# Kernel optimization log

Measured on AMD Instinct MI355X. Metric: run time of the kernel, lower is better.

## Reference

```python
import jax, jax.numpy as jnp
import numpy as np

B, C, L = 8, 512, 2048   # batch, input_dim (channels), sequence length
H = 8                    # multihead_cnt
K = 3                    # kernel_dim
DH = C // H              # per-head dim = 64
SCALE = 1.0 / float(np.sqrt(C))  # module divides by sqrt(input_dim), not sqrt(head_dim)


def _conv1d(x, w, b):
    # x: [B, C, L], w: [C_out, C_in, K], padding=1 keeps L
    y = jax.lax.conv_general_dilated(x, w, window_strides=(1,), padding=[(1, 1)],
                                     dimension_numbers=('NCH', 'OIH', 'NCH'))
    return y + b[None, :, None]


def setup_inputs() -> dict:
    key = jax.random.key(0)
    ks = jax.random.split(key, 7)
    x = jax.random.normal(ks[0], (B, C, L), dtype=jnp.float32)
    # xavier_normal_ std for Conv1d weight [C, C, K]: sqrt(2 / (fan_in + fan_out)), fan = C*K
    std = float(np.sqrt(2.0 / (C * K + C * K)))
    inp = {'x': x}
    for i in range(3):  # conv_cnt = 3 -> q, k, v convolutions
        inp[f'w{i}'] = jax.random.normal(ks[1 + 2 * i], (C, C, K), dtype=jnp.float32) * std
        inp[f'b{i}'] = jax.random.normal(ks[2 + 2 * i], (C,), dtype=jnp.float32) * 0.01
    return inp


def reference(x, w0, b0, w1, b1, w2, b2):
    # q, k, v projections via Conv1d (padding preserves length)
    q = _conv1d(x, w0, b0)  # [B, C, L]
    k = _conv1d(x, w1, b1)
    v = _conv1d(x, w2, b2)
    # torch.chunk along dim 1 == contiguous reshape into heads
    qh = q.reshape(B, H, DH, L)
    kh = k.reshape(B, H, DH, L)
    vh = v.reshape(B, H, DH, L)
    # scores = q^T k / sqrt(input_dim)  -> [B, H, L, L]
    scores = jnp.einsum('bhdl,bhdm->bhlm', qh, kh) * SCALE
    att = jax.nn.softmax(scores, axis=-1)
    # out = (att @ v^T)^T -> [B, H, DH, L]
    out = jnp.einsum('bhlm,bhdm->bhdl', att, vh)
    return out.reshape(B, C, L)
```

## Files before the change

kernel.cpp:

```cpp
#include <hip/hip_runtime.h>
#include <hip/hip_bf16.h>
#include <cstdint>

typedef unsigned short u16;
typedef short v8s __attribute__((ext_vector_type(8)));
typedef float v4f __attribute__((ext_vector_type(4)));
typedef u16 u16x8 __attribute__((ext_vector_type(8)));
typedef u16 u16x4 __attribute__((ext_vector_type(4)));

static constexpr int Bb = 8, Cc = 512, Ll = 2048, Hh = 8, Dh = 64;

__device__ __forceinline__ float bf2f(u16 u){
  unsigned x = ((unsigned)u) << 16; float f; __builtin_memcpy(&f, &x, 4); return f;
}
__device__ __forceinline__ u16 f2bf(float f){
  unsigned x; __builtin_memcpy(&x, &f, 4);
  x = (x + 0x7fffu + ((x >> 16) & 1u)) >> 16; return (u16)x;
}

__device__ __forceinline__ void async_cp16(const u16* g, u16* l){
  __builtin_amdgcn_global_load_lds(
      (const __attribute__((address_space(1))) unsigned int*)g,
      (__attribute__((address_space(3))) unsigned int*)l, 16, 0, 0);
}

#if __has_builtin(__builtin_amdgcn_exp2f)
#define EXP2F(x) __builtin_amdgcn_exp2f(x)
#else
#define EXP2F(x) exp2f(x)
#endif

__global__ __launch_bounds__(256) void detect_dtype(const u16* __restrict__ x, unsigned* __restrict__ flag){
  __shared__ int cnt;
  if (threadIdx.x == 0) cnt = 0;
  __syncthreads();
  int sane = 0;
  for (int i = threadIdx.x; i < 4096; i += 256){
    unsigned e = (x[2 * i] >> 7) & 0xFFu;
    sane += (e >= 90u && e <= 160u) ? 1 : 0;
  }
  atomicAdd(&cnt, sane);
  __syncthreads();
  if (threadIdx.x == 0) *flag = (cnt < 2458) ? 1u : 0u;
}

__global__ __launch_bounds__(256) void transpose_pad(const void* __restrict__ xv, const unsigned* __restrict__ flagp,
                                                     u16* __restrict__ xT){
  int b = blockIdx.z, ci0 = blockIdx.y * 64, l0 = blockIdx.x * 64;
  __shared__ u16 tb[64 * 72];
  const unsigned isf32 = *flagp;
  int t = threadIdx.x;
  int row = t >> 3, seg = t & 7;
  if (isf32){
    const float* xf = (const float*)xv;
    #pragma unroll
    for (int rnd = 0; rnd < 2; rnd++){
      int ci = row + rnd * 32;
      size_t off = ((size_t)(b * Cc + ci0 + ci)) * Ll + l0 + seg * 8;
      v4f a = *(const v4f*)(xf + off);
      v4f c4 = *(const v4f*)(xf + off + 4);
      #pragma unroll
      for (int j = 0; j < 4; j++) tb[(seg * 8 + j) * 72 + ci] = f2bf(a[j]);
      #pragma unroll
      for (int j = 0; j < 4; j++) tb[(seg * 8 + 4 + j) * 72 + ci] = f2bf(c4[j]);
    }
  } else {
    const u16* x = (const u16*)xv;
    #pragma unroll
    for (int rnd = 0; rnd < 2; rnd++){
      int ci = row + rnd * 32;
      u16x8 v = *(const u16x8*)(x + ((size_t)(b * Cc + ci0 + ci)) * Ll + l0 + seg * 8);
      #pragma unroll
      for (int j = 0; j < 8; j++) tb[(seg * 8 + j) * 72 + ci] = v[j];
    }
  }
  __syncthreads();
  #pragma unroll
  for (int rnd = 0; rnd < 2; rnd++){
    int l = row + rnd * 32;
    u16x8 v = *(const u16x8*)&tb[l * 72 + seg * 8];
    *(u16x8*)(xT + ((size_t)b * 2050 + 1 + l0 + l) * Cc + ci0 + seg * 8) = v;
  }
}

__global__ __launch_bounds__(256) void pack_w(const void* __restrict__ w0, const void* __restrict__ w1,
                                              const void* __restrict__ w2, const unsigned* __restrict__ flagp,
                                              u16* __restrict__ wp){
  int g = blockIdx.x * 256 + threadIdx.x;
  int ci = g & 511, co = (g >> 9) & 511, kc = g >> 18;
  int conv = kc / 3, k = kc - conv * 3;
  const void* w = (conv == 0) ? w0 : ((conv == 1) ? w1 : w2);
  size_t idx = (size_t)co * 1536 + ci * 3 + k;
  if (*flagp) wp[g] = f2bf(((const float*)w)[idx]);
  else        wp[g] = ((const u16*)w)[idx];
}

__global__ __launch_bounds__(256) void pack_b(const void* __restrict__ b0, const void* __restrict__ b1,
                                              const void* __restrict__ b2, const unsigned* __restrict__ flagp,
                                              u16* __restrict__ bb){
  int g = blockIdx.x * 256 + threadIdx.x;
  if (g >= 1536) return;
  int conv = g >> 9, c = g & 511;
  const void* bsrc = (conv == 0) ? b0 : ((conv == 1) ? b1 : b2);
  if (*flagp) bb[g] = f2bf(((const float*)bsrc)[c]);
  else        bb[g] = ((const u16*)bsrc)[c];
}

__global__ __launch_bounds__(256) void conv_gemm_fused(const u16* __restrict__ wp, const u16* __restrict__ xT,
                                                       const u16* __restrict__ bb, u16* __restrict__ qT,
                                                       u16* __restrict__ kT, u16* __restrict__ vN){
  int b = blockIdx.y, bx = blockIdx.x;
  int mt = bx >> 4, nt = bx & 15;
  int m0 = mt * 128, n0 = nt * 128;
  int conv = m0 >> 9;
  int co0 = m0 & 511;
  __shared__ u16 lA[3 * 128 * 32];
  __shared__ u16 lB[130 * 32];
  int t = threadIdx.x, wave = t >> 6, lane = t & 63, quad = lane >> 4, lid = lane & 15;
  int wm = (wave >> 1) * 64, wn = (wave & 1) * 64;
  v4f acc[4][4] = {};
  const size_t xbase = (size_t)b * 2050 * Cc;

  for (int it = 0; it < 16; it++){
    int ci0 = it << 5;
    #pragma unroll
    for (int r = 0; r < 2; r++){
      int e = (r * 256 + t) * 8;
      int row = e >> 5, cio = e & 31;
      async_cp16(xT + xbase + (size_t)(n0 + row) * 512 + ci0 + cio, &lB[e]);
    }
    #pragma unroll
    for (int r = 0; r < 6; r++){
      int e = (r * 256 + t) * 8;
      int ks = e >> 12, rem = e & 4095, row = rem >> 5, cio = rem & 31;
      async_cp16(wp + ((size_t)((conv * 3 + ks) * 512 + co0 + row)) * 512 + ci0 + cio, &lA[e]);
    }
    if (t < 8){
      int hr = 128 + (t >> 2), cio = (t & 3) * 8;
      u16x8 hv = *(const u16x8*)(xT + xbase + (size_t)(n0 + hr) * 512 + ci0 + cio);
      *(u16x8*)&lB[hr * 32 + cio] = hv;
    }
    __syncthreads();
    #pragma unroll
    for (int ks = 0; ks < 3; ks++){
      v8s aF[4], bF[4];
      #pragma unroll
      for (int i = 0; i < 4; i++) aF[i] = *(const v8s*)&lA[ks * 4096 + (wm + i * 16 + lid) * 32 + quad * 8];
      #pragma unroll
      for (int j = 0; j < 4; j++) bF[j] = *(const v8s*)&lB[(wn + j * 16 + lid + ks) * 32 + quad * 8];
      #pragma unroll
      for (int i = 0; i < 4; i++)
        #pragma unroll
        for (int j = 0; j < 4; j++)
          acc[i][j] = __builtin_amdgcn_mfma_f32_16x16x32_bf16(aF[i], bF[j], acc[i][j], 0, 0, 0);
    }
    __syncthreads();
  }

  const float qsc = (float)(1.4426950408889634 / 22.627416997969522);
  #pragma unroll
  for (int i = 0; i < 4; i++){
    int cog = m0 + wm + i * 16 + quad * 4;
    float bv[4];
    #pragma unroll
    for (int r = 0; r < 4; r++) bv[r] = bf2f(bb[cog + r]);
    #pragma unroll
    for (int j = 0; j < 4; j++){
      int l = n0 + wn + j * 16 + lid;
      if (conv < 2){
        int co = cog & 511;
        u16* dst = (conv == 0) ? qT : kT;
        u16x4 pk;
        #pragma unroll
        for (int r = 0; r < 4; r++){
          float v = acc[i][j][r] + bv[r];
          if (conv == 0) v *= qsc;
          pk[r] = f2bf(v);
        }
        *(u16x4*)(dst + ((((size_t)b * Hh + (co >> 6)) * Ll + l) << 6) + (co & 63)) = pk;
      } else {
        int co = cog - 1024;
        #pragma unroll
        for (int r = 0; r < 4; r++)
          vN[(((size_t)b * Cc + co + r) << 11) + l] = f2bf(acc[i][j][r] + bv[r]);
      }
    }
  }
}

__global__ __launch_bounds__(256) void attn_kernel(const u16* __restrict__ qT, const u16* __restrict__ kT,
                                                   const u16* __restrict__ vN, const unsigned* __restrict__ flagp,
                                                   void* __restrict__ outv){
  int bhx = blockIdx.x;
  int b = bhx >> 3, h = bhx & 7, l0 = blockIdx.y * 128;
  int t = threadIdx.x, w = t >> 6, lane = t & 63, quad = lane >> 4, lid = lane & 15;
  __shared__ u16 kls[128 * 72];
  __shared__ u16 vls[64 * 136];
  __shared__ float al[128];
  const unsigned isf32 = *flagp;
  const size_t bh = (size_t)b * Hh + h;

  v8s qF[2][2];
  #pragma unroll
  for (int ci = 0; ci < 2; ci++)
    #pragma unroll
    for (int ks = 0; ks < 2; ks++)
      qF[ci][ks] = *(const v8s*)(qT + ((bh * Ll) + l0 + w * 32 + ci * 16 + lid) * 64 + ks * 32 + quad * 8);

  v4f o[2][4] = {};
  float lsum[2] = {0.f, 0.f};

  for (int mt = 0; mt < 16; mt++){
    int m0 = mt * 128;
    {
      int row = t >> 3, seg = t & 7;
      #pragma unroll
      for (int rnd = 0; rnd < 4; rnd++){
        int m = row + rnd * 32;
        int slot = (m & ~31) | ((m & 4) << 2) | ((m & 24) >> 1) | (m & 3);
        u16x8 v = *(const u16x8*)(kT + (bh * Ll + m0 + m) * 64 + seg * 8);
        *(u16x8*)&kls[slot * 72 + seg * 8] = v;
      }
      int vrow = t >> 4, vseg = t & 15;
      #pragma unroll
      for (int rnd = 0; rnd < 4; rnd++){
        int d = vrow + rnd * 16;
        u16x8 v = *(const u16x8*)(vN + ((size_t)(b * Cc + h * Dh + d)) * Ll + m0 + vseg * 8);
        *(u16x8*)&vls[d * 136 + vseg * 8] = v;
      }
    }
    __syncthreads();

    v4f s[4][2][2] = {};
    #pragma unroll
    for (int ks = 0; ks < 2; ks++){
      v8s aF[4][2];
      #pragma unroll
      for (int c = 0; c < 4; c++)
        #pragma unroll
        for (int tt = 0; tt < 2; tt++)
          aF[c][tt] = *(const v8s*)&kls[(c * 32 + tt * 16 + lid) * 72 + ks * 32 + quad * 8];
      #pragma unroll
      for (int c = 0; c < 4; c++)
        #pragma unroll
        for (int tt = 0; tt < 2; tt++){
          s[c][tt][0] = __builtin_amdgcn_mfma_f32_16x16x32_bf16(aF[c][tt], qF[0][ks], s[c][tt][0], 0, 0, 0);
          s[c][tt][1] = __builtin_amdgcn_mfma_f32_16x16x32_bf16(aF[c][tt], qF[1][ks], s[c][tt][1], 0, 0, 0);
        }
    }

    #pragma unroll
    for (int c = 0; c < 4; c++){
      v8s aP[2];
      #pragma unroll
      for (int ci = 0; ci < 2; ci++){
        float p[8];
        #pragma unroll
        for (int tt = 0; tt < 2; tt++)
          #pragma unroll
          for (int r = 0; r < 4; r++){
            float e = EXP2F(s[c][tt][ci][r]);
            p[tt * 4 + r] = e;
            lsum[ci] += e;
          }
        unsigned u[4];
        #pragma unroll
        for (int k2 = 0; k2 < 4; k2++){
          __hip_bfloat162 hb = __float22bfloat162_rn(make_float2(p[2 * k2], p[2 * k2 + 1]));
          __builtin_memcpy(&u[k2], &hb, 4);
        }
        __builtin_memcpy(&aP[ci], u, 16);
      }
      v8s bV[4];
      #pragma unroll
      for (int df = 0; df < 4; df++)
        bV[df] = *(const v8s*)&vls[(df * 16 + lid) * 136 + c * 32 + quad * 8];
      #pragma unroll
      for (int ci = 0; ci < 2; ci++)
        #pragma unroll
        for (int df = 0; df < 4; df++)
          o[ci][df] = __builtin_amdgcn_mfma_f32_16x16x32_bf16(aP[ci], bV[df], o[ci][df], 0, 0, 0);
    }
    __syncthreads();
  }

  #pragma unroll
  for (int ci = 0; ci < 2; ci++){
    lsum[ci] += __shfl_xor(lsum[ci], 16);
    lsum[ci] += __shfl_xor(lsum[ci], 32);
  }
  if (quad == 0){
    al[w * 32 + lid] = 1.f / lsum[0];
    al[w * 32 + 16 + lid] = 1.f / lsum[1];
  }
  __syncthreads();
  #pragma unroll
  for (int lf = 0; lf < 2; lf++){
    v4f nv = *(const v4f*)&al[w * 32 + lf * 16 + quad * 4];
    #pragma unroll
    for (int df = 0; df < 4; df++){
      int d = df * 16 + lid;
      int l = l0 + w * 32 + lf * 16 + quad * 4;
      size_t ofs = (((bh << 6) + d) << 11) + l;
      if (isf32){
        v4f st;
        #pragma unroll
        for (int r = 0; r < 4; r++) st[r] = o[lf][df][r] * nv[r];
        *(v4f*)((float*)outv + ofs) = st;
      } else {
        u16x4 pk;
        #pragma unroll
        for (int r = 0; r < 4; r++) pk[r] = f2bf(o[lf][df][r] * nv[r]);
        *(u16x4*)((u16*)outv + ofs) = pk;
      }
    }
  }
}

extern "C" void kernel_launch(void* const* d_in, const int* in_sizes, int n_in,
                              void* d_out, int out_size, void* d_ws, size_t ws_size,
                              hipStream_t stream){
  const void* x  = d_in[0];
  const void* w0 = d_in[1];
  const void* b0 = d_in[2];
  const void* w1 = d_in[3];
  const void* b1 = d_in[4];
  const void* w2 = d_in[5];
  const void* b2 = d_in[6];
  u16* ws = (u16*)d_ws;
  unsigned* flag = (unsigned*)ws;
  u16* xT = ws + 64;
  u16* wp = xT + (size_t)8 * 2050 * 512;
  u16* bb = wp + (size_t)9 * 512 * 512;
  u16* qT = bb + 1536;
  u16* kT = qT + (size_t)8 * 8 * 2048 * 64;
  u16* vN = kT + (size_t)8 * 8 * 2048 * 64;

  detect_dtype<<<1, 256, 0, stream>>>((const u16*)x, flag);
  (void)hipMemsetAsync(xT, 0, (size_t)8 * 2050 * 512 * 2, stream);
  transpose_pad<<<dim3(32, 8, 8), 256, 0, stream>>>(x, flag, xT);
  pack_w<<<dim3(9 * 512 * 512 / 256), 256, 0, stream>>>(w0, w1, w2, flag, wp);
  pack_b<<<dim3(6), 256, 0, stream>>>(b0, b1, b2, flag, bb);
  conv_gemm_fused<<<dim3(192, 8), 256, 0, stream>>>(wp, xT, bb, qT, kT, vN);
  attn_kernel<<<dim3(64, 16), 256, 0, stream>>>(qT, kT, vN, flag, d_out);
}
```

Baseline: 321.8 us.

## Widen conv GEMM tile, async-load attention K/V, compute row sums via MFMA

Several changes land at once. The full-buffer memset is replaced by zeroing only the two pad rows inside transpose_pad, and the weight and bias pack kernels are merged into one launch. The conv GEMM N-tile doubles to 256 and the V output is staged through LDS for coalesced stores. The attention kernel loads K and V with global_load_lds async copies and computes softmax row sums with an extra MFMA against a ones vector instead of scalar adds and shuffles. This cuts launches, redundant memory traffic and VALU work, at the cost of higher register pressure in the GEMM and extra MFMA issue in attention.

```diff
diff --git a/kernel.cpp b/kernel.cpp
--- a/kernel.cpp
+++ b/kernel.cpp
@@ -81,50 +81,59 @@
     u16x8 v = *(const u16x8*)&tb[l * 72 + seg * 8];
     *(u16x8*)(xT + ((size_t)b * 2050 + 1 + l0 + l) * Cc + ci0 + seg * 8) = v;
   }
-}
-
-__global__ __launch_bounds__(256) void pack_w(const void* __restrict__ w0, const void* __restrict__ w1,
-                                              const void* __restrict__ w2, const unsigned* __restrict__ flagp,
-                                              u16* __restrict__ wp){
+  if (blockIdx.x == 0 && t < 8){
+    u16x8 z = {};
+    *(u16x8*)(xT + ((size_t)b * 2050 + 0) * Cc + ci0 + t * 8) = z;
+  }
+  if (blockIdx.x == 31 && t < 8){
+    u16x8 z = {};
+    *(u16x8*)(xT + ((size_t)b * 2050 + 2049) * Cc + ci0 + t * 8) = z;
+  }
+}
+
+__global__ __launch_bounds__(256) void pack_wb(const void* __restrict__ w0, const void* __restrict__ w1,
+                                               const void* __restrict__ w2, const void* __restrict__ b0,
+                                               const void* __restrict__ b1, const void* __restrict__ b2,
+                                               const unsigned* __restrict__ flagp,
+                                               u16* __restrict__ wp, u16* __restrict__ bb){
   int g = blockIdx.x * 256 + threadIdx.x;
-  int ci = g & 511, co = (g >> 9) & 511, kc = g >> 18;
-  int conv = kc / 3, k = kc - conv * 3;
-  const void* w = (conv == 0) ? w0 : ((conv == 1) ? w1 : w2);
-  size_t idx = (size_t)co * 1536 + ci * 3 + k;
-  if (*flagp) wp[g] = f2bf(((const float*)w)[idx]);
-  else        wp[g] = ((const u16*)w)[idx];
-}
-
-__global__ __launch_bounds__(256) void pack_b(const void* __restrict__ b0, const void* __restrict__ b1,
-                                              const void* __restrict__ b2, const unsigned* __restrict__ flagp,
-                                              u16* __restrict__ bb){
-  int g = blockIdx.x * 256 + threadIdx.x;
-  if (g >= 1536) return;
-  int conv = g >> 9, c = g & 511;
-  const void* bsrc = (conv == 0) ? b0 : ((conv == 1) ? b1 : b2);
-  if (*flagp) bb[g] = f2bf(((const float*)bsrc)[c]);
-  else        bb[g] = ((const u16*)bsrc)[c];
+  const unsigned isf32 = *flagp;
+  if (g < 9 * 512 * 512){
+    int ci = g & 511, co = (g >> 9) & 511, kc = g >> 18;
+    int conv = kc / 3, k = kc - conv * 3;
+    const void* w = (conv == 0) ? w0 : ((conv == 1) ? w1 : w2);
+    size_t idx = (size_t)co * 1536 + ci * 3 + k;
+    wp[g] = isf32 ? f2bf(((const float*)w)[idx]) : ((const u16*)w)[idx];
+  } else {
+    int g2 = g - 9 * 512 * 512;
+    if (g2 < 1536){
+      int conv = g2 >> 9, c = g2 & 511;
+      const void* bsrc = (conv == 0) ? b0 : ((conv == 1) ? b1 : b2);
+      bb[g2] = isf32 ? f2bf(((const float*)bsrc)[c]) : ((const u16*)bsrc)[c];
+    }
+  }
 }
 
 __global__ __launch_bounds__(256) void conv_gemm_fused(const u16* __restrict__ wp, const u16* __restrict__ xT,
                                                        const u16* __restrict__ bb, u16* __restrict__ qT,
                                                        u16* __restrict__ kT, u16* __restrict__ vN){
   int b = blockIdx.y, bx = blockIdx.x;
-  int mt = bx >> 4, nt = bx & 15;
-  int m0 = mt * 128, n0 = nt * 128;
+  int mt = bx >> 3, nt = bx & 7;
+  int m0 = mt * 128, n0 = nt * 256;
   int conv = m0 >> 9;
   int co0 = m0 & 511;
-  __shared__ u16 lA[3 * 128 * 32];
-  __shared__ u16 lB[130 * 32];
+  __shared__ u16 smem[12288 + 8256];
+  u16* lA = smem;
+  u16* lB = smem + 12288;
   int t = threadIdx.x, wave = t >> 6, lane = t & 63, quad = lane >> 4, lid = lane & 15;
-  int wm = (wave >> 1) * 64, wn = (wave & 1) * 64;
-  v4f acc[4][4] = {};
+  int wm = (wave >> 1) * 64, wn = (wave & 1) * 128;
+  v4f acc[4][8] = {};
   const size_t xbase = (size_t)b * 2050 * Cc;
 
   for (int it = 0; it < 16; it++){
     int ci0 = it << 5;
     #pragma unroll
-    for (int r = 0; r < 2; r++){
+    for (int r = 0; r < 4; r++){
       int e = (r * 256 + t) * 8;
       int row = e >> 5, cio = e & 31;
       async_cp16(xT + xbase + (size_t)(n0 + row) * 512 + ci0 + cio, &lB[e]);
@@ -136,40 +145,40 @@
       async_cp16(wp + ((size_t)((conv * 3 + ks) * 512 + co0 + row)) * 512 + ci0 + cio, &lA[e]);
     }
     if (t < 8){
-      int hr = 128 + (t >> 2), cio = (t & 3) * 8;
+      int hr = 256 + (t >> 2), cio = (t & 3) * 8;
       u16x8 hv = *(const u16x8*)(xT + xbase + (size_t)(n0 + hr) * 512 + ci0 + cio);
       *(u16x8*)&lB[hr * 32 + cio] = hv;
     }
     __syncthreads();
     #pragma unroll
     for (int ks = 0; ks < 3; ks++){
-      v8s aF[4], bF[4];
+      v8s aF[4], bF[8];
       #pragma unroll
       for (int i = 0; i < 4; i++) aF[i] = *(const v8s*)&lA[ks * 4096 + (wm + i * 16 + lid) * 32 + quad * 8];
       #pragma unroll
-      for (int j = 0; j < 4; j++) bF[j] = *(const v8s*)&lB[(wn + j * 16 + lid + ks) * 32 + quad * 8];
+      for (int j = 0; j < 8; j++) bF[j] = *(const v8s*)&lB[(wn + j * 16 + lid + ks) * 32 + quad * 8];
       #pragma unroll
       for (int i = 0; i < 4; i++)
         #pragma unroll
-        for (int j = 0; j < 4; j++)
+        for (int j = 0; j < 8; j++)
           acc[i][j] = __builtin_amdgcn_mfma_f32_16x16x32_bf16(aF[i], bF[j], acc[i][j], 0, 0, 0);
     }
     __syncthreads();
   }
 
   const float qsc = (float)(1.4426950408889634 / 22.627416997969522);
-  #pragma unroll
-  for (int i = 0; i < 4; i++){
-    int cog = m0 + wm + i * 16 + quad * 4;
-    float bv[4];
-    #pragma unroll
-    for (int r = 0; r < 4; r++) bv[r] = bf2f(bb[cog + r]);
-    #pragma unroll
-    for (int j = 0; j < 4; j++){
-      int l = n0 + wn + j * 16 + lid;
-      if (conv < 2){
-        int co = cog & 511;
-        u16* dst = (conv == 0) ? qT : kT;
+  if (conv < 2){
+    u16* dst = (conv == 0) ? qT : kT;
+    #pragma unroll
+    for (int i = 0; i < 4; i++){
+      int cog = m0 + wm + i * 16 + quad * 4;
+      float bv[4];
+      #pragma unroll
+      for (int r = 0; r < 4; r++) bv[r] = bf2f(bb[cog + r]);
+      int co = cog & 511;
+      #pragma unroll
+      for (int j = 0; j < 8; j++){
+        int l = n0 + wn + j * 16 + lid;
         u16x4 pk;
         #pragma unroll
         for (int r = 0; r < 4; r++){
@@ -178,11 +187,36 @@
           pk[r] = f2bf(v);
         }
         *(u16x4*)(dst + ((((size_t)b * Hh + (co >> 6)) * Ll + l) << 6) + (co & 63)) = pk;
-      } else {
-        int co = cog - 1024;
-        #pragma unroll
-        for (int r = 0; r < 4; r++)
-          vN[(((size_t)b * Cc + co + r) << 11) + l] = f2bf(acc[i][j][r] + bv[r]);
+      }
+    }
+  } else {
+    u16* scr = smem;
+    #pragma unroll
+    for (int cs = 0; cs < 2; cs++){
+      __syncthreads();
+      #pragma unroll
+      for (int i = 0; i < 4; i++){
+        int cog = m0 + wm + i * 16 + quad * 4;
+        float bv[4];
+        #pragma unroll
+        for (int r = 0; r < 4; r++) bv[r] = bf2f(bb[cog + r]);
+        #pragma unroll
+        for (int j = 0; j < 4; j++){
+          int jj = cs * 4 + j;
+          int lcl = (wave & 1) * 64 + j * 16 + lid;
+          #pragma unroll
+          for (int r = 0; r < 4; r++)
+            scr[(wm + i * 16 + quad * 4 + r) * 130 + lcl] = f2bf(acc[i][jj][r] + bv[r]);
+        }
+      }
+      __syncthreads();
+      int row = t & 127, half = t >> 7;
+      int co = co0 + row;
+      size_t gb = (((size_t)b * Cc + co) << 11) + n0 + half * 128 + cs * 64;
+      #pragma unroll
+      for (int s = 0; s < 8; s++){
+        u16x8 vv = *(const u16x8*)&scr[row * 130 + half * 64 + s * 8];
+        *(u16x8*)(vN + gb + s * 8) = vv;
       }
     }
   }
@@ -196,9 +230,25 @@
   int t = threadIdx.x, w = t >> 6, lane = t & 63, quad = lane >> 4, lid = lane & 15;
   __shared__ u16 kls[128 * 72];
   __shared__ u16 vls[64 * 136];
-  __shared__ float al[128];
   const unsigned isf32 = *flagp;
   const size_t bh = (size_t)b * Hh + h;
+
+  int kadd[5], vadd[5];
+  bool kval[5], vval[5];
+  #pragma unroll
+  for (int r = 0; r < 5; r++){
+    int e = (r * 256 + t) * 8;
+    kval[r] = e < 128 * 72;
+    int slot = e / 72, off = e - slot * 72;
+    int s5 = slot & 31;
+    int m = (slot & ~31) | (((s5 >> 2) & 1) << 3) | (((s5 >> 3) & 1) << 4) | (((s5 >> 4) & 1) << 2) | (s5 & 3);
+    kadd[r] = m * 64 + (off < 64 ? off : 0);
+    vval[r] = e < 64 * 136;
+    int d = e / 136, voff = e - d * 136;
+    vadd[r] = d * Ll + (voff < 128 ? voff : 0);
+  }
+  const u16* kTb = kT + bh * Ll * 64;
+  const u16* vNb = vN + ((size_t)(b * Cc + h * Dh)) * Ll;
 
   v8s qF[2][2];
   #pragma unroll
@@ -207,28 +257,20 @@
     for (int ks = 0; ks < 2; ks++)
       qF[ci][ks] = *(const v8s*)(qT + ((bh * Ll) + l0 + w * 32 + ci * 16 + lid) * 64 + ks * 32 + quad * 8);
 
+  const v8s onesF = {0x3F80, 0x3F80, 0x3F80, 0x3F80, 0x3F80, 0x3F80, 0x3F80, 0x3F80};
   v4f o[2][4] = {};
-  float lsum[2] = {0.f, 0.f};
+  v4f o1[2] = {};
 
   for (int mt = 0; mt < 16; mt++){
     int m0 = mt * 128;
-    {
-      int row = t >> 3, seg = t & 7;
-      #pragma unroll
-      for (int rnd = 0; rnd < 4; rnd++){
-        int m = row + rnd * 32;
-        int slot = (m & ~31) | ((m & 4) << 2) | ((m & 24) >> 1) | (m & 3);
-        u16x8 v = *(const u16x8*)(kT + (bh * Ll + m0 + m) * 64 + seg * 8);
-        *(u16x8*)&kls[slot * 72 + seg * 8] = v;
-      }
-      int vrow = t >> 4, vseg = t & 15;
-      #pragma unroll
-      for (int rnd = 0; rnd < 4; rnd++){
-        int d = vrow + rnd * 16;
-        u16x8 v = *(const u16x8*)(vN + ((size_t)(b * Cc + h * Dh + d)) * Ll + m0 + vseg * 8);
-        *(u16x8*)&vls[d * 136 + vseg * 8] = v;
-      }
-    }
+    const u16* kt = kTb + (size_t)m0 * 64;
+    const u16* vt = vNb + m0;
+    #pragma unroll
+    for (int r = 0; r < 5; r++)
+      if (kval[r]) async_cp16(kt + kadd[r], &kls[(r * 256 + t) * 8]);
+    #pragma unroll
+    for (int r = 0; r < 5; r++)
+      if (vval[r]) async_cp16(vt + vadd[r], &vls[(r * 256 + t) * 8]);
     __syncthreads();
 
     v4f s[4][2][2] = {};
@@ -258,11 +300,8 @@
         #pragma unroll
         for (int tt = 0; tt < 2; tt++)
           #pragma unroll
-          for (int r = 0; r < 4; r++){
-            float e = EXP2F(s[c][tt][ci][r]);
-            p[tt * 4 + r] = e;
-            lsum[ci] += e;
-          }
+          for (int r = 0; r < 4; r++)
+            p[tt * 4 + r] = EXP2F(s[c][tt][ci][r]);
         unsigned u[4];
         #pragma unroll
         for (int k2 = 0; k2 < 4; k2++){
@@ -276,27 +315,21 @@
       for (int df = 0; df < 4; df++)
         bV[df] = *(const v8s*)&vls[(df * 16 + lid) * 136 + c * 32 + quad * 8];
       #pragma unroll
-      for (int ci = 0; ci < 2; ci++)
+      for (int ci = 0; ci < 2; ci++){
         #pragma unroll
         for (int df = 0; df < 4; df++)
           o[ci][df] = __builtin_amdgcn_mfma_f32_16x16x32_bf16(aP[ci], bV[df], o[ci][df], 0, 0, 0);
+        o1[ci] = __builtin_amdgcn_mfma_f32_16x16x32_bf16(aP[ci], onesF, o1[ci], 0, 0, 0);
+      }
     }
     __syncthreads();
   }
 
-  #pragma unroll
-  for (int ci = 0; ci < 2; ci++){
-    lsum[ci] += __shfl_xor(lsum[ci], 16);
-    lsum[ci] += __shfl_xor(lsum[ci], 32);
-  }
-  if (quad == 0){
-    al[w * 32 + lid] = 1.f / lsum[0];
-    al[w * 32 + 16 + lid] = 1.f / lsum[1];
-  }
-  __syncthreads();
   #pragma unroll
   for (int lf = 0; lf < 2; lf++){
-    v4f nv = *(const v4f*)&al[w * 32 + lf * 16 + quad * 4];
+    v4f nv;
+    #pragma unroll
+    for (int r = 0; r < 4; r++) nv[r] = 1.f / o1[lf][r];
     #pragma unroll
     for (int df = 0; df < 4; df++){
       int d = df * 16 + lid;
@@ -337,10 +370,8 @@
   u16* vN = kT + (size_t)8 * 8 * 2048 * 64;
 
   detect_dtype<<<1, 256, 0, stream>>>((const u16*)x, flag);
-  (void)hipMemsetAsync(xT, 0, (size_t)8 * 2050 * 512 * 2, stream);
   transpose_pad<<<dim3(32, 8, 8), 256, 0, stream>>>(x, flag, xT);
-  pack_w<<<dim3(9 * 512 * 512 / 256), 256, 0, stream>>>(w0, w1, w2, flag, wp);
-  pack_b<<<dim3(6), 256, 0, stream>>>(b0, b1, b2, flag, bb);
-  conv_gemm_fused<<<dim3(192, 8), 256, 0, stream>>>(wp, xT, bb, qT, kT, vN);
+  pack_wb<<<dim3(9 * 512 * 512 / 256 + 6), 256, 0, stream>>>(w0, w1, w2, b0, b1, b2, flag, wp, bb);
+  conv_gemm_fused<<<dim3(96, 8), 256, 0, stream>>>(wp, xT, bb, qT, kT, vN);
   attn_kernel<<<dim3(64, 16), 256, 0, stream>>>(qT, kT, vN, flag, d_out);
 }
```

Measured after the change: 297.5 us. 7.6% less time.
